# Kernel optimization log

Measured on AMD Instinct MI355X. Metric: run time of the kernel, lower is better.

The kernel has to match this reference:

```python
import jax, jax.numpy as jnp
import numpy as np

D_MODEL = 1024
NUM_HEADS = 16
SEQ_LEN = 2048
HEAD_DIM = D_MODEL // NUM_HEADS


def _rope_thetas(seq_len, head_dim):
    # Standard RoPE angles: theta[s, j] = s * 10000^(-2j/d), j in [0, d/2)
    d_half = head_dim // 2
    pos = jnp.arange(seq_len, dtype=jnp.float32)
    freqs = 1.0 / jnp.power(10000.0, jnp.arange(0, head_dim, 2, dtype=jnp.float32) / head_dim)
    thetas = pos[:, None] * freqs[None, :]  # [S, d_half]
    return jnp.cos(thetas), jnp.sin(thetas)


def _apply_rope(x, cos, sin):
    # x: [B, H, S, D]; rotate consecutive pairs (x_{2i}, x_{2i+1}) by theta_i
    b, h, s, d = x.shape
    xp = x.reshape(b, h, s, d // 2, 2)
    x1, x2 = xp[..., 0], xp[..., 1]
    c = cos[None, None, :, :]
    sn = sin[None, None, :, :]
    o1 = x1 * c - x2 * sn
    o2 = x1 * sn + x2 * c
    return jnp.stack([o1, o2], axis=-1).reshape(b, h, s, d)


def setup_inputs() -> dict:
    key = jax.random.key(0)
    k_x, k_wqkv, k_bqkv, k_wo, k_bo = jax.random.split(key, 5)
    lim_qkv = 1.0 / np.sqrt(D_MODEL)
    x = jax.random.normal(k_x, (2, SEQ_LEN, D_MODEL), dtype=jnp.float32)
    w_qkv = jax.random.uniform(k_wqkv, (3 * D_MODEL, D_MODEL), jnp.float32, -lim_qkv, lim_qkv)
    b_qkv = jax.random.uniform(k_bqkv, (3 * D_MODEL,), jnp.float32, -lim_qkv, lim_qkv)
    w_out = jax.random.uniform(k_wo, (D_MODEL, D_MODEL), jnp.float32, -lim_qkv, lim_qkv)
    b_out = jax.random.uniform(k_bo, (D_MODEL,), jnp.float32, -lim_qkv, lim_qkv)
    return {"x": x, "w_qkv": w_qkv, "b_qkv": b_qkv, "w_out": w_out, "b_out": b_out}


def reference(x, w_qkv, b_qkv, w_out, b_out):
    B, S, D = x.shape
    H, Dh = NUM_HEADS, D // NUM_HEADS
    qkv = x @ w_qkv.T + b_qkv  # [B, S, 3D]
    q, k, v = jnp.split(qkv, 3, axis=-1)
    # [B, S, D] -> [B, H, S, Dh]
    q = q.reshape(B, S, H, Dh).transpose(0, 2, 1, 3)
    k = k.reshape(B, S, H, Dh).transpose(0, 2, 1, 3)
    v = v.reshape(B, S, H, Dh).transpose(0, 2, 1, 3)
    cos, sin = _rope_thetas(S, Dh)
    q = _apply_rope(q, cos, sin)
    k = _apply_rope(k, cos, sin)
    scores = jnp.einsum('bhqd,bhkd->bhqk', q, k) / jnp.sqrt(jnp.float32(Dh))
    causal = jnp.tril(jnp.ones((S, S), dtype=bool))
    scores = jnp.where(causal[None, None, :, :], scores, jnp.float32(-jnp.inf))
    attn = jax.nn.softmax(scores, axis=-1)
    o = jnp.einsum('bhqk,bhkd->bhqd', attn, v)  # [B, H, S, Dh]
    o = o.transpose(0, 2, 1, 3).reshape(B, S, D)
    return o @ w_out.T + b_out
```

## Files before the change

kernel.cpp:

```cpp
#include <hip/hip_runtime.h>
#include <stdint.h>

#define S_LEN 2048
#define NH 16
#define DM 1024
#define HD 64
#define NB 2
#define TOK (NB * S_LEN)

typedef __attribute__((ext_vector_type(8))) short short8v;
typedef __attribute__((ext_vector_type(4))) float f32x4;
typedef __attribute__((ext_vector_type(2))) unsigned int u32x2;
typedef unsigned short u16;
typedef unsigned int u32;

__device__ __forceinline__ float bf2f(u16 u) {
    u32 x = ((u32)u) << 16;
    return __builtin_bit_cast(float, x);
}
__device__ __forceinline__ u16 f2bf(float f) {
    u32 u = __builtin_bit_cast(u32, f);
    return (u16)((u + 0x7FFFu + ((u >> 16) & 1u)) >> 16);
}
__device__ __forceinline__ u32 cvtpk(float lo, float hi) {
    u32 r;
    asm("v_cvt_pk_bf16_f32 %0, %1, %2" : "=v"(r) : "v"(lo), "v"(hi));
    return r;
}

__device__ __forceinline__ void gld_lds16(const void* g, void* lds_base_uniform) {
    auto gp = (const __attribute__((address_space(1))) u32*)(uintptr_t)g;
    auto lp = (__attribute__((address_space(3))) u32*)(uintptr_t)(u32)(uintptr_t)lds_base_uniform;
    __builtin_amdgcn_global_load_lds(gp, lp, 16, 0, 0);
}

__global__ void detect_dtype(const u32* __restrict__ xw, int* __restrict__ flag) {
    __shared__ int cnt[4];
    const int t = threadIdx.x;
    int c = 0;
#pragma unroll
    for (int j = 0; j < 16; ++j) {
        const u32 wd = xw[(t * 16 + j) * 64];
        const u32 e = (wd >> 7) & 0xFF;
        c += (e >= 0x58 && e <= 0x98) ? 1 : 0;
    }
#pragma unroll
    for (int off = 1; off < 64; off <<= 1) c += __shfl_xor(c, off);
    if ((t & 63) == 0) cnt[t >> 6] = c;
    __syncthreads();
    if (t == 0) flag[0] = (cnt[0] + cnt[1] + cnt[2] + cnt[3] >= 2600) ? 1 : 0;
}

#define XCH (TOK * DM / 8)
#define WQCH (3 * DM * DM / 8)
#define WOCH (DM * DM / 8)
__global__ __launch_bounds__(256) void convert_all(
    const void* __restrict__ xs, const void* __restrict__ wqs, const void* __restrict__ wos,
    u16* __restrict__ xd, u16* __restrict__ wqd, u16* __restrict__ wod,
    const int* __restrict__ flagp) {
    int i = blockIdx.x * 256 + threadIdx.x;
    const void* src;
    u16* dst;
    if (i < XCH) {
        src = xs; dst = xd;
    } else if (i < XCH + WQCH) {
        src = wqs; dst = wqd; i -= XCH;
    } else {
        src = wos; dst = wod; i -= XCH + WQCH;
    }
    if (flagp[0]) {
        ((short8v*)dst)[i] = ((const short8v*)src)[i];
    } else {
        const f32x4 v0 = ((const f32x4*)src)[2 * i];
        const f32x4 v1 = ((const f32x4*)src)[2 * i + 1];
        short8v o;
#pragma unroll
        for (int q = 0; q < 4; ++q) o[q] = (short)f2bf(v0[q]);
#pragma unroll
        for (int q = 0; q < 4; ++q) o[4 + q] = (short)f2bf(v1[q]);
        ((short8v*)dst)[i] = o;
    }
}

__global__ __launch_bounds__(256) void gemm_bt_bias(
    const u16* __restrict__ A, const u16* __restrict__ Bt,
    const void* __restrict__ biasv, void* __restrict__ Cv,
    int M, int N, int K, const int* __restrict__ flagp, int out_flagged) {
    __shared__ __align__(16) u16 lA[3][128 * 32];
    __shared__ __align__(16) u16 lB[3][128 * 32];
    const int fl = flagp[0];
    const int fo = out_flagged ? fl : 1;

    const int tid = threadIdx.x;
    const int w = __builtin_amdgcn_readfirstlane(tid >> 6);
    const int lane = tid & 63;
    const int quad = lane >> 4;
    const int l16 = lane & 15;
    const int bm = blockIdx.y * 128;
    const int bn = blockIdx.x * 128;
    const int wm = (w >> 1) * 64;
    const int wn = (w & 1) * 64;

    f32x4 acc[4][4];
#pragma unroll
    for (int i = 0; i < 4; ++i)
#pragma unroll
        for (int j = 0; j < 4; ++j) acc[i][j] = {0.f, 0.f, 0.f, 0.f};

    const int kiters = K >> 5;
#define GEMM_STAGE(kk, buf)                                                            \
    {                                                                                  \
        _Pragma("unroll") for (int c = 0; c < 2; ++c) {                                \
            const int chunk = w * 2 + c;                                               \
            const int off = chunk * 1024 + lane * 16;                                  \
            const int m_ = off >> 6;                                                   \
            const int kb_ = off & 63;                                                  \
            gld_lds16((const char*)(A + (size_t)(bm + m_) * K + (kk) * 32) + kb_,      \
                      (char*)&lA[buf][0] + chunk * 1024);                              \
            gld_lds16((const char*)(Bt + (size_t)(bn + m_) * K + (kk) * 32) + kb_,     \
                      (char*)&lB[buf][0] + chunk * 1024);                              \
        }                                                                              \
    }

    GEMM_STAGE(0, 0);
    if (kiters > 1) GEMM_STAGE(1, 1);
    int cur = 0;
    for (int kk = 0; kk < kiters; ++kk) {
        if (kk + 1 < kiters) {
            asm volatile("s_waitcnt vmcnt(4)" ::: "memory");
        } else {
            asm volatile("s_waitcnt vmcnt(0)" ::: "memory");
        }
        __builtin_amdgcn_s_barrier();
        if (kk + 2 < kiters) {
            const int nb = (cur + 2 >= 3) ? cur - 1 : cur + 2;
            GEMM_STAGE(kk + 2, nb);
        }

        short8v af[4], bf[4];
#pragma unroll
        for (int t = 0; t < 4; ++t) {
            af[t] = *(const short8v*)&lA[cur][(wm + t * 16 + l16) * 32 + quad * 8];
            bf[t] = *(const short8v*)&lB[cur][(wn + t * 16 + l16) * 32 + quad * 8];
        }
        __builtin_amdgcn_s_setprio(1);
#pragma unroll
        for (int i = 0; i < 4; ++i)
#pragma unroll
            for (int j = 0; j < 4; ++j)
                acc[i][j] = __builtin_amdgcn_mfma_f32_16x16x32_bf16(bf[j], af[i], acc[i][j], 0, 0, 0);
        __builtin_amdgcn_s_setprio(0);
        cur = (cur == 2) ? 0 : cur + 1;
    }
#undef GEMM_STAGE

#pragma unroll
    for (int j = 0; j < 4; ++j) {
        const int n0 = bn + wn + j * 16 + quad * 4;
        float bv0, bv1, bv2, bv3;
        if (fl) {
            const u32x2 bw = *(const u32x2*)((const u16*)biasv + n0);
            bv0 = bf2f((u16)(bw.x & 0xffff));
            bv1 = bf2f((u16)(bw.x >> 16));
            bv2 = bf2f((u16)(bw.y & 0xffff));
            bv3 = bf2f((u16)(bw.y >> 16));
        } else {
            const f32x4 bw = *(const f32x4*)((const float*)biasv + n0);
            bv0 = bw[0]; bv1 = bw[1]; bv2 = bw[2]; bv3 = bw[3];
        }
#pragma unroll
        for (int i = 0; i < 4; ++i) {
            const size_t base = (size_t)(bm + wm + i * 16 + l16) * N + n0;
            const float v0 = acc[i][j][0] + bv0, v1 = acc[i][j][1] + bv1;
            const float v2 = acc[i][j][2] + bv2, v3 = acc[i][j][3] + bv3;
            if (fo) {
                u32x2 ov;
                ov.x = cvtpk(v0, v1);
                ov.y = cvtpk(v2, v3);
                *(u32x2*)((u16*)Cv + base) = ov;
            } else {
                f32x4 ov = {v0, v1, v2, v3};
                *(f32x4*)((float*)Cv + base) = ov;
            }
        }
    }
}

__global__ __launch_bounds__(256) void rope_vt(
    const u16* __restrict__ qkv, u16* __restrict__ qws, u16* __restrict__ kws,
    u16* __restrict__ vTo) {
    __shared__ u16 tile[64 * 65];
    if (blockIdx.x < 8192) {
        const int idx = blockIdx.x * 256 + threadIdx.x;
        const int i = idx & 31;
        const int h = (idx >> 5) & 15;
        const int s = (idx >> 9) & 2047;
        const int b = idx >> 20;
        const u16* src = qkv + ((size_t)(b * S_LEN + s)) * (3 * DM) + h * HD + 2 * i;
        const u32 qp = *(const u32*)(src);
        const u32 kp = *(const u32*)(src + DM);
        const float q1 = bf2f((u16)qp), q2 = bf2f((u16)(qp >> 16));
        const float k1 = bf2f((u16)kp), k2 = bf2f((u16)(kp >> 16));
        const float freq = expf(-(float)(2 * i) * 0.14391156831212787f);
        const float th = (float)s * freq;
        float sn, cs;
        sincosf(th, &sn, &cs);
        const float oq1 = q1 * cs - q2 * sn, oq2 = q1 * sn + q2 * cs;
        const float ok1 = k1 * cs - k2 * sn, ok2 = k1 * sn + k2 * cs;
        const size_t dst = ((size_t)((b * NH + h) * S_LEN + s)) * HD + 2 * i;
        *(u32*)(qws + dst) = (u32)f2bf(oq1) | ((u32)f2bf(oq2) << 16);
        *(u32*)(kws + dst) = (u32)f2bf(ok1) | ((u32)f2bf(ok2) << 16);
    } else {
        const int bid = blockIdx.x - 8192;
        const int s0 = (bid & 31) * 64;
        const int h = (bid >> 5) & 15, b = bid >> 9;
        const int t = threadIdx.x;
#pragma unroll
        for (int it = 0; it < 16; ++it) {
            const int e = t + 256 * it;
            const int sl = e >> 6, d = e & 63;
            tile[sl * 65 + d] =
                qkv[((size_t)(b * S_LEN + s0 + sl)) * (3 * DM) + 2 * DM + h * HD + d];
        }
        __syncthreads();
#pragma unroll
        for (int it = 0; it < 16; ++it) {
            const int e = t + 256 * it;
            const int d = e >> 6, sl = e & 63;
            vTo[((size_t)((b * NH + h) * HD + d)) * S_LEN + s0 + sl] = tile[sl * 65 + d];
        }
    }
}

__global__ __launch_bounds__(256, 4) void attn_kernel(
    const u16* __restrict__ qws, const u16* __restrict__ kws,
    const u16* __restrict__ vT, u16* __restrict__ ows) {
    __shared__ __align__(16) u16 kl[2][64 * 64];
    __shared__ __align__(16) u16 vl[64 * 64];
    __shared__ __align__(16) u32 pl32[4][16 * 36];
    const int t = threadIdx.x;
    const int w = __builtin_amdgcn_readfirstlane(t >> 6);
    const int lane = t & 63;
    const int quad = lane >> 4;
    const int l16 = lane & 15;

    const int id = blockIdx.x;
    const int g = id & 31;
    const int qb = 31 - (id >> 5);
    const int h = g & 15, b = g >> 4;
    const int q0 = qb * 64 + w * 16;

    const size_t bh = (size_t)(b * NH + h);
    const u16* qbp = qws + bh * (size_t)S_LEN * HD;
    const u16* kb = kws + bh * (size_t)S_LEN * HD;
    const u16* vb = vT + bh * (size_t)HD * S_LEN;

    const int r0 = lane >> 3;
    const int srcc = (lane & 7) ^ r0;
    const int xorb = (l16 & 7) << 4;

    short8v qf[2];
#pragma unroll
    for (int hf = 0; hf < 2; ++hf)
        qf[hf] = *(const short8v*)(qbp + (size_t)(q0 + l16) * HD + hf * 32 + quad * 8);

    f32x4 oaccT[4];
#pragma unroll
    for (int d = 0; d < 4; ++d) oaccT[d] = {0.f, 0.f, 0.f, 0.f};
    float mrow = -__builtin_inff();
    float lrow = 0.f;

#pragma unroll
    for (int s = 0; s < 2; ++s) {
        const int row = w * 8 + s * 32 + r0;
        gld_lds16(kb + (size_t)row * HD + srcc * 8, (char*)&kl[0][0] + w * 1024 + s * 4096);
    }

    int cur = 0;
    for (int kt = 0; kt <= qb; ++kt) {
        __syncthreads();
#pragma unroll
        for (int s = 0; s < 2; ++s) {
            const int row = w * 8 + s * 32 + r0;
            gld_lds16(vb + (size_t)row * S_LEN + kt * 64 + srcc * 8,
                      (char*)&vl[0] + w * 1024 + s * 4096);
        }
        if (kt < qb) {
#pragma unroll
            for (int s = 0; s < 2; ++s) {
                const int row = w * 8 + s * 32 + r0;
                gld_lds16(kb + (size_t)((kt + 1) * 64 + row) * HD + srcc * 8,
                          (char*)&kl[cur ^ 1][0] + w * 1024 + s * 4096);
            }
        }
        const char* Kb = (const char*)&kl[cur][0];

        f32x4 s4[4];
        __builtin_amdgcn_s_setprio(1);
#pragma unroll
        for (int sub = 0; sub < 4; ++sub) {
            const int lin = (sub * 16 + l16) * 128 + quad * 16;
            const short8v k0 = *(const short8v*)(Kb + (lin ^ xorb));
            const short8v k1 = *(const short8v*)(Kb + ((lin + 64) ^ xorb));
            f32x4 a = {0.f, 0.f, 0.f, 0.f};
            a = __builtin_amdgcn_mfma_f32_16x16x32_bf16(k0, qf[0], a, 0, 0, 0);
            a = __builtin_amdgcn_mfma_f32_16x16x32_bf16(k1, qf[1], a, 0, 0, 0);
            s4[sub] = a;
        }
        __builtin_amdgcn_s_setprio(0);
        float sv[16];
#pragma unroll
        for (int sub = 0; sub < 4; ++sub)
#pragma unroll
            for (int r = 0; r < 4; ++r) sv[sub * 4 + r] = s4[sub][r] * 0.125f;
        if (kt == qb) {
            const int qloc = w * 16 + l16;
#pragma unroll
            for (int sub = 0; sub < 4; ++sub)
#pragma unroll
                for (int r = 0; r < 4; ++r)
                    if (sub * 16 + quad * 4 + r > qloc) sv[sub * 4 + r] = -__builtin_inff();
        }
        float a0 = fmaxf(sv[0], sv[1]), a1 = fmaxf(sv[2], sv[3]);
        float a2 = fmaxf(sv[4], sv[5]), a3 = fmaxf(sv[6], sv[7]);
        float a4 = fmaxf(sv[8], sv[9]), a5 = fmaxf(sv[10], sv[11]);
        float a6 = fmaxf(sv[12], sv[13]), a7 = fmaxf(sv[14], sv[15]);
        a0 = fmaxf(a0, a1); a2 = fmaxf(a2, a3);
        a4 = fmaxf(a4, a5); a6 = fmaxf(a6, a7);
        a0 = fmaxf(a0, a2); a4 = fmaxf(a4, a6);
        float mx = fmaxf(a0, a4);
        mx = fmaxf(mx, __shfl_xor(mx, 16));
        mx = fmaxf(mx, __shfl_xor(mx, 32));
        const float mnew = fmaxf(mrow, mx);
        const float alpha = __expf(mrow - mnew);
        mrow = mnew;
        float p[16];
#pragma unroll
        for (int i = 0; i < 16; ++i) p[i] = __expf(sv[i] - mnew);
        float b0 = p[0] + p[1], b1 = p[2] + p[3], b2 = p[4] + p[5], b3 = p[6] + p[7];
        float b4 = p[8] + p[9], b5 = p[10] + p[11], b6 = p[12] + p[13], b7 = p[14] + p[15];
        b0 += b1; b2 += b3; b4 += b5; b6 += b7;
        b0 += b2; b4 += b6;
        float ps = b0 + b4;
        ps += __shfl_xor(ps, 16);
        ps += __shfl_xor(ps, 32);
        lrow = lrow * alpha + ps;
#pragma unroll
        for (int d = 0; d < 4; ++d) oaccT[d] *= alpha;
        u32* prow = &pl32[w][l16 * 36];
#pragma unroll
        for (int sub = 0; sub < 4; ++sub) {
            u32x2 pw;
            pw.x = cvtpk(p[sub * 4 + 0], p[sub * 4 + 1]);
            pw.y = cvtpk(p[sub * 4 + 2], p[sub * 4 + 3]);
            *(u32x2*)&prow[sub * 8 + quad * 2] = pw;
        }
        asm volatile("s_waitcnt lgkmcnt(0)" ::: "memory");
        if (kt < qb) {
            asm volatile("s_waitcnt vmcnt(2)" ::: "memory");
        } else {
            asm volatile("s_waitcnt vmcnt(0)" ::: "memory");
        }
        __builtin_amdgcn_s_barrier();
        asm volatile("" ::: "memory");
        __builtin_amdgcn_s_setprio(1);
#pragma unroll
        for (int c2 = 0; c2 < 2; ++c2) {
            const short8v pf = *(const short8v*)&pl32[w][l16 * 36 + c2 * 16 + quad * 4];
#pragma unroll
            for (int d = 0; d < 4; ++d) {
                const int lin = (d * 16 + l16) * 128 + c2 * 64 + quad * 16;
                const short8v vfd = *(const short8v*)((const char*)&vl[0] + (lin ^ xorb));
                oaccT[d] = __builtin_amdgcn_mfma_f32_16x16x32_bf16(vfd, pf, oaccT[d], 0, 0, 0);
            }
        }
        __builtin_amdgcn_s_setprio(0);
        cur ^= 1;
    }

    const float inv = 1.0f / lrow;
    const size_t rowbase = ((size_t)(b * S_LEN + q0 + l16)) * DM + h * HD;
#pragma unroll
    for (int df = 0; df < 4; ++df) {
        const int d0 = df * 16 + quad * 4;
        u32x2 ov;
        ov.x = cvtpk(oaccT[df][0] * inv, oaccT[df][1] * inv);
        ov.y = cvtpk(oaccT[df][2] * inv, oaccT[df][3] * inv);
        *(u32x2*)(ows + rowbase + d0) = ov;
    }
}

extern "C" void kernel_launch(void* const* d_in, const int* in_sizes, int n_in,
                              void* d_out, int out_size, void* d_ws, size_t ws_size,
                              hipStream_t stream) {
    const void* x = d_in[0];
    const void* w_qkv = d_in[1];
    const void* b_qkv = d_in[2];
    const void* w_out = d_in[3];
    const void* b_out = d_in[4];

    int* flag = (int*)d_ws;
    u16* qkv = (u16*)d_ws + 8;
    u16* qws = qkv + (size_t)TOK * 3 * DM;
    u16* kws = qws + (size_t)NB * NH * S_LEN * HD;
    u16* vT = kws + (size_t)NB * NH * S_LEN * HD;
    u16* woutb = vT + (size_t)NB * NH * HD * S_LEN;
    u16* ows = qkv;
    u16* xb = qws;
    u16* wqkvb = kws;

    detect_dtype<<<1, 256, 0, stream>>>((const u32*)x, flag);
    convert_all<<<(XCH + WQCH + WOCH) / 256, 256, 0, stream>>>(
        x, w_qkv, w_out, xb, wqkvb, woutb, flag);

    gemm_bt_bias<<<dim3(3 * DM / 128, TOK / 128), 256, 0, stream>>>(
        xb, wqkvb, b_qkv, qkv, TOK, 3 * DM, DM, flag, 0);
    rope_vt<<<8192 + 1024, 256, 0, stream>>>(qkv, qws, kws, vT);
    attn_kernel<<<dim3(32 * 32), 256, 0, stream>>>(qws, kws, vT, ows);
    gemm_bt_bias<<<dim3(DM / 128, TOK / 128), 256, 0, stream>>>(
        ows, woutb, b_out, d_out, TOK, DM, DM, flag, 1);
}
```

Baseline: 215.5 us.

## Fuse RoPE and V transpose into QKV GEMM epilogue with precomputed trig table

Removes the separate rope_vt kernel. The QKV GEMM epilogue now applies RoPE to Q and K using a cos/sin table precomputed inside the convert kernel, and writes head-major layouts directly. For the V column blocks the MFMA operands are swapped so the accumulator is transposed and V^T can be stored without a shared-memory transpose. This avoids writing and re-reading the full QKV intermediate, at the cost of a more complex epilogue with scattered, less coalesced stores and per-element table loads.

```diff
diff --git a/kernel.cpp b/kernel.cpp
--- a/kernel.cpp
+++ b/kernel.cpp
@@ -54,11 +54,23 @@
 #define XCH (TOK * DM / 8)
 #define WQCH (3 * DM * DM / 8)
 #define WOCH (DM * DM / 8)
+#define CONVTOT (XCH + WQCH + WOCH)
+#define TABN (S_LEN * 32)
 __global__ __launch_bounds__(256) void convert_all(
     const void* __restrict__ xs, const void* __restrict__ wqs, const void* __restrict__ wos,
     u16* __restrict__ xd, u16* __restrict__ wqd, u16* __restrict__ wod,
-    const int* __restrict__ flagp) {
+    float* __restrict__ tab, const int* __restrict__ flagp) {
     int i = blockIdx.x * 256 + threadIdx.x;
+    if (i >= CONVTOT) {
+        const int e = i - CONVTOT;
+        const int s = e >> 5, ii = e & 31;
+        const float freq = expf(-(float)ii * 0.2878231366242557f);
+        float sn, cs;
+        sincosf((float)s * freq, &sn, &cs);
+        tab[e * 2] = cs;
+        tab[e * 2 + 1] = sn;
+        return;
+    }
     const void* src;
     u16* dst;
     if (i < XCH) {
@@ -85,7 +97,9 @@
 __global__ __launch_bounds__(256) void gemm_bt_bias(
     const u16* __restrict__ A, const u16* __restrict__ Bt,
     const void* __restrict__ biasv, void* __restrict__ Cv,
-    int M, int N, int K, const int* __restrict__ flagp, int out_flagged) {
+    int M, int N, int K, const int* __restrict__ flagp, int out_flagged,
+    int mode, u16* __restrict__ qws, u16* __restrict__ kws,
+    u16* __restrict__ vT, const float* __restrict__ tab) {
     __shared__ __align__(16) u16 lA[3][128 * 32];
     __shared__ __align__(16) u16 lB[3][128 * 32];
     const int fl = flagp[0];
@@ -100,6 +114,7 @@
     const int bn = blockIdx.x * 128;
     const int wm = (w >> 1) * 64;
     const int wn = (w & 1) * 64;
+    const bool vblk = (mode == 1) && (blockIdx.x >= 16);
 
     f32x4 acc[4][4];
 #pragma unroll
@@ -144,90 +159,111 @@
             bf[t] = *(const short8v*)&lB[cur][(wn + t * 16 + l16) * 32 + quad * 8];
         }
         __builtin_amdgcn_s_setprio(1);
-#pragma unroll
-        for (int i = 0; i < 4; ++i)
-#pragma unroll
-            for (int j = 0; j < 4; ++j)
-                acc[i][j] = __builtin_amdgcn_mfma_f32_16x16x32_bf16(bf[j], af[i], acc[i][j], 0, 0, 0);
+        if (vblk) {
+#pragma unroll
+            for (int i = 0; i < 4; ++i)
+#pragma unroll
+                for (int j = 0; j < 4; ++j)
+                    acc[i][j] =
+                        __builtin_amdgcn_mfma_f32_16x16x32_bf16(af[i], bf[j], acc[i][j], 0, 0, 0);
+        } else {
+#pragma unroll
+            for (int i = 0; i < 4; ++i)
+#pragma unroll
+                for (int j = 0; j < 4; ++j)
+                    acc[i][j] =
+                        __builtin_amdgcn_mfma_f32_16x16x32_bf16(bf[j], af[i], acc[i][j], 0, 0, 0);
+        }
         __builtin_amdgcn_s_setprio(0);
         cur = (cur == 2) ? 0 : cur + 1;
     }
 #undef GEMM_STAGE
 
-#pragma unroll
-    for (int j = 0; j < 4; ++j) {
-        const int n0 = bn + wn + j * 16 + quad * 4;
-        float bv0, bv1, bv2, bv3;
-        if (fl) {
-            const u32x2 bw = *(const u32x2*)((const u16*)biasv + n0);
-            bv0 = bf2f((u16)(bw.x & 0xffff));
-            bv1 = bf2f((u16)(bw.x >> 16));
-            bv2 = bf2f((u16)(bw.y & 0xffff));
-            bv3 = bf2f((u16)(bw.y >> 16));
-        } else {
-            const f32x4 bw = *(const f32x4*)((const float*)biasv + n0);
-            bv0 = bw[0]; bv1 = bw[1]; bv2 = bw[2]; bv3 = bw[3];
-        }
-#pragma unroll
-        for (int i = 0; i < 4; ++i) {
-            const size_t base = (size_t)(bm + wm + i * 16 + l16) * N + n0;
-            const float v0 = acc[i][j][0] + bv0, v1 = acc[i][j][1] + bv1;
-            const float v2 = acc[i][j][2] + bv2, v3 = acc[i][j][3] + bv3;
-            if (fo) {
+    if (mode == 0) {
+#pragma unroll
+        for (int j = 0; j < 4; ++j) {
+            const int n0 = bn + wn + j * 16 + quad * 4;
+            float bv0, bv1, bv2, bv3;
+            if (fl) {
+                const u32x2 bw = *(const u32x2*)((const u16*)biasv + n0);
+                bv0 = bf2f((u16)(bw.x & 0xffff));
+                bv1 = bf2f((u16)(bw.x >> 16));
+                bv2 = bf2f((u16)(bw.y & 0xffff));
+                bv3 = bf2f((u16)(bw.y >> 16));
+            } else {
+                const f32x4 bw = *(const f32x4*)((const float*)biasv + n0);
+                bv0 = bw[0]; bv1 = bw[1]; bv2 = bw[2]; bv3 = bw[3];
+            }
+#pragma unroll
+            for (int i = 0; i < 4; ++i) {
+                const size_t base = (size_t)(bm + wm + i * 16 + l16) * N + n0;
+                const float v0 = acc[i][j][0] + bv0, v1 = acc[i][j][1] + bv1;
+                const float v2 = acc[i][j][2] + bv2, v3 = acc[i][j][3] + bv3;
+                if (fo) {
+                    u32x2 ov;
+                    ov.x = cvtpk(v0, v1);
+                    ov.y = cvtpk(v2, v3);
+                    *(u32x2*)((u16*)Cv + base) = ov;
+                } else {
+                    f32x4 ov = {v0, v1, v2, v3};
+                    *(f32x4*)((float*)Cv + base) = ov;
+                }
+            }
+        }
+    } else if (vblk) {
+#pragma unroll
+        for (int j = 0; j < 4; ++j) {
+            const int n = bn + wn + j * 16 + l16;
+            const float bv = fl ? bf2f(((const u16*)biasv)[n]) : ((const float*)biasv)[n];
+            const int vcol = n - 2048;
+            const int hh = vcol >> 6, d = vcol & 63;
+#pragma unroll
+            for (int i = 0; i < 4; ++i) {
+                const int m0 = bm + wm + i * 16 + quad * 4;
+                const int bb = m0 >> 11, s0 = m0 & 2047;
                 u32x2 ov;
-                ov.x = cvtpk(v0, v1);
-                ov.y = cvtpk(v2, v3);
-                *(u32x2*)((u16*)Cv + base) = ov;
+                ov.x = cvtpk(acc[i][j][0] + bv, acc[i][j][1] + bv);
+                ov.y = cvtpk(acc[i][j][2] + bv, acc[i][j][3] + bv);
+                *(u32x2*)(vT + ((size_t)((bb * NH + hh) * HD + d)) * S_LEN + s0) = ov;
+            }
+        }
+    } else {
+        const bool isq = (blockIdx.x < 8);
+        u16* outp = isq ? qws : kws;
+#pragma unroll
+        for (int j = 0; j < 4; ++j) {
+            const int n0 = bn + wn + j * 16 + quad * 4;
+            float bv0, bv1, bv2, bv3;
+            if (fl) {
+                const u32x2 bw = *(const u32x2*)((const u16*)biasv + n0);
+                bv0 = bf2f((u16)(bw.x & 0xffff));
+                bv1 = bf2f((u16)(bw.x >> 16));
+                bv2 = bf2f((u16)(bw.y & 0xffff));
+                bv3 = bf2f((u16)(bw.y >> 16));
             } else {
-                f32x4 ov = {v0, v1, v2, v3};
-                *(f32x4*)((float*)Cv + base) = ov;
-            }
-        }
-    }
-}
-
-__global__ __launch_bounds__(256) void rope_vt(
-    const u16* __restrict__ qkv, u16* __restrict__ qws, u16* __restrict__ kws,
-    u16* __restrict__ vTo) {
-    __shared__ u16 tile[64 * 65];
-    if (blockIdx.x < 8192) {
-        const int idx = blockIdx.x * 256 + threadIdx.x;
-        const int i = idx & 31;
-        const int h = (idx >> 5) & 15;
-        const int s = (idx >> 9) & 2047;
-        const int b = idx >> 20;
-        const u16* src = qkv + ((size_t)(b * S_LEN + s)) * (3 * DM) + h * HD + 2 * i;
-        const u32 qp = *(const u32*)(src);
-        const u32 kp = *(const u32*)(src + DM);
-        const float q1 = bf2f((u16)qp), q2 = bf2f((u16)(qp >> 16));
-        const float k1 = bf2f((u16)kp), k2 = bf2f((u16)(kp >> 16));
-        const float freq = expf(-(float)(2 * i) * 0.14391156831212787f);
-        const float th = (float)s * freq;
-        float sn, cs;
-        sincosf(th, &sn, &cs);
-        const float oq1 = q1 * cs - q2 * sn, oq2 = q1 * sn + q2 * cs;
-        const float ok1 = k1 * cs - k2 * sn, ok2 = k1 * sn + k2 * cs;
-        const size_t dst = ((size_t)((b * NH + h) * S_LEN + s)) * HD + 2 * i;
-        *(u32*)(qws + dst) = (u32)f2bf(oq1) | ((u32)f2bf(oq2) << 16);
-        *(u32*)(kws + dst) = (u32)f2bf(ok1) | ((u32)f2bf(ok2) << 16);
-    } else {
-        const int bid = blockIdx.x - 8192;
-        const int s0 = (bid & 31) * 64;
-        const int h = (bid >> 5) & 15, b = bid >> 9;
-        const int t = threadIdx.x;
-#pragma unroll
-        for (int it = 0; it < 16; ++it) {
-            const int e = t + 256 * it;
-            const int sl = e >> 6, d = e & 63;
-            tile[sl * 65 + d] =
-                qkv[((size_t)(b * S_LEN + s0 + sl)) * (3 * DM) + 2 * DM + h * HD + d];
-        }
-        __syncthreads();
-#pragma unroll
-        for (int it = 0; it < 16; ++it) {
-            const int e = t + 256 * it;
-            const int d = e >> 6, sl = e & 63;
-            vTo[((size_t)((b * NH + h) * HD + d)) * S_LEN + s0 + sl] = tile[sl * 65 + d];
+                const f32x4 bw = *(const f32x4*)((const float*)biasv + n0);
+                bv0 = bw[0]; bv1 = bw[1]; bv2 = bw[2]; bv3 = bw[3];
+            }
+            const int nc = n0 & 1023;
+            const int hh = nc >> 6;
+            const int d0 = nc & 63;
+            const int i0 = d0 >> 1;
+#pragma unroll
+            for (int i = 0; i < 4; ++i) {
+                const int m = bm + wm + i * 16 + l16;
+                const int bb = m >> 11, s = m & 2047;
+                const f32x4 cs4 = *(const f32x4*)(tab + ((size_t)s * 32 + i0) * 2);
+                const float v0 = acc[i][j][0] + bv0, v1 = acc[i][j][1] + bv1;
+                const float v2 = acc[i][j][2] + bv2, v3 = acc[i][j][3] + bv3;
+                const float o0 = v0 * cs4[0] - v1 * cs4[1];
+                const float o1 = v0 * cs4[1] + v1 * cs4[0];
+                const float o2 = v2 * cs4[2] - v3 * cs4[3];
+                const float o3 = v2 * cs4[3] + v3 * cs4[2];
+                u32x2 ov;
+                ov.x = cvtpk(o0, o1);
+                ov.y = cvtpk(o2, o3);
+                *(u32x2*)(outp + ((size_t)((bb * NH + hh) * S_LEN + s)) * HD + d0) = ov;
+            }
         }
     }
 }
@@ -400,23 +436,24 @@
     const void* b_out = d_in[4];
 
     int* flag = (int*)d_ws;
-    u16* qkv = (u16*)d_ws + 8;
-    u16* qws = qkv + (size_t)TOK * 3 * DM;
+    u16* xb = (u16*)d_ws + 8;
+    u16* wqkvb = xb + (size_t)TOK * DM;
+    u16* woutb = wqkvb + (size_t)3 * DM * DM;
+    u16* qws = woutb + (size_t)DM * DM;
     u16* kws = qws + (size_t)NB * NH * S_LEN * HD;
     u16* vT = kws + (size_t)NB * NH * S_LEN * HD;
-    u16* woutb = vT + (size_t)NB * NH * HD * S_LEN;
-    u16* ows = qkv;
-    u16* xb = qws;
-    u16* wqkvb = kws;
+    u16* ows = vT + (size_t)NB * NH * HD * S_LEN;
+    float* tab = (float*)(ows + (size_t)TOK * DM);
 
     detect_dtype<<<1, 256, 0, stream>>>((const u32*)x, flag);
-    convert_all<<<(XCH + WQCH + WOCH) / 256, 256, 0, stream>>>(
-        x, w_qkv, w_out, xb, wqkvb, woutb, flag);
+    convert_all<<<(CONVTOT + TABN) / 256, 256, 0, stream>>>(
+        x, w_qkv, w_out, xb, wqkvb, woutb, tab, flag);
 
     gemm_bt_bias<<<dim3(3 * DM / 128, TOK / 128), 256, 0, stream>>>(
-        xb, wqkvb, b_qkv, qkv, TOK, 3 * DM, DM, flag, 0);
-    rope_vt<<<8192 + 1024, 256, 0, stream>>>(qkv, qws, kws, vT);
+        xb, wqkvb, b_qkv, nullptr, TOK, 3 * DM, DM, flag, 0,
+        1, qws, kws, vT, tab);
     attn_kernel<<<dim3(32 * 32), 256, 0, stream>>>(qws, kws, vT, ows);
     gemm_bt_bias<<<dim3(DM / 128, TOK / 128), 256, 0, stream>>>(
-        ows, woutb, b_out, d_out, TOK, DM, DM, flag, 1);
-}
+        ows, woutb, b_out, d_out, TOK, DM, DM, flag, 1,
+        0, nullptr, nullptr, nullptr, nullptr);
+}
```

New measurement: 216.1 us. About the same (+0.3%).
